# Optimization experiments

Hardware: AMD Instinct MI355X
Metric: run time of the kernel (lower is better)

Reference implementation:

```python
import jax, jax.numpy as jnp
import numpy as np

B, T, E = 2, 2048, 1024
H = 16            # num_heads (global in source repo)
D = E // H        # head_len
LN_EPS = 1e-5


def setup_inputs() -> dict:
    key = jax.random.key(0)
    ks = jax.random.split(key, 12)
    s = lambda fan_in: 1.0 / np.sqrt(fan_in)
    return {
        "x":     jax.random.normal(ks[0], (B, T, E), jnp.float32),
        "ln1_g": jnp.ones((E,), jnp.float32),
        "ln1_b": jnp.zeros((E,), jnp.float32),
        "Wq":    jax.random.normal(ks[1], (E, E), jnp.float32) * s(E),
        "Wk":    jax.random.normal(ks[2], (E, E), jnp.float32) * s(E),
        "Wv":    jax.random.normal(ks[3], (E, E), jnp.float32) * s(E),
        "Wo":    jax.random.normal(ks[4], (E, E), jnp.float32) * s(E),
        "bo":    jnp.zeros((E,), jnp.float32),
        "ln2_g": jnp.ones((E,), jnp.float32),
        "ln2_b": jnp.zeros((E,), jnp.float32),
        "W1":    jax.random.normal(ks[5], (E, 4 * E), jnp.float32) * s(E),
        "b1":    jnp.zeros((4 * E,), jnp.float32),
        "W2":    jax.random.normal(ks[6], (4 * E, E), jnp.float32) * s(4 * E),
        "b2":    jnp.zeros((E,), jnp.float32),
    }


def _layernorm(x, g, b):
    mu = jnp.mean(x, axis=-1, keepdims=True)
    var = jnp.mean(jnp.square(x - mu), axis=-1, keepdims=True)
    return (x - mu) * jax.lax.rsqrt(var + LN_EPS) * g + b


def _attention(x, Wq, Wk, Wv, Wo, bo):
    b, t, e = x.shape
    q = (x @ Wq).reshape(b, t, H, D)
    k = (x @ Wk).reshape(b, t, H, D)
    v = (x @ Wv).reshape(b, t, H, D)
    scores = jnp.einsum("bqhd,bkhd->bhqk", q, k) / np.sqrt(D).astype(np.float32)
    causal = jnp.tril(jnp.ones((t, t), bool))
    scores = jnp.where(causal, scores, -jnp.inf)
    attn = jax.nn.softmax(scores, axis=-1)
    out = jnp.einsum("bhqk,bkhd->bqhd", attn, v).reshape(b, t, e)
    return out @ Wo + bo


def reference(x, ln1_g, ln1_b, Wq, Wk, Wv, Wo, bo, ln2_g, ln2_b, W1, b1, W2, b2):
    # pre-norm attention + residual (dropout=0 / eval mode)
    x = x + _attention(_layernorm(x, ln1_g, ln1_b), Wq, Wk, Wv, Wo, bo)
    # pre-norm MLP + residual
    h = _layernorm(x, ln2_g, ln2_b)
    h = jax.nn.relu(h @ W1 + b1) @ W2 + b2
    return x + h
```

## Files before the change

kernel.cpp:

```cpp
#include <hip/hip_runtime.h>
#include <cmath>
#include <cstdint>
#include <cstddef>

typedef __bf16 bf16_t;
typedef __bf16 bf16x8 __attribute__((ext_vector_type(8)));
typedef float  f32x4  __attribute__((ext_vector_type(4)));

#define B_   2
#define T_   2048
#define E_   1024
#define H_   16
#define D_   64
#define FF_  4096
#define NROW (B_ * T_)
#define QS_  (3 * E_)
#define NTI  (T_ / 64)

__global__ __launch_bounds__(256) void ln_kernel(
    const float* __restrict__ x, const float* __restrict__ g,
    const float* __restrict__ bta, bf16_t* __restrict__ out)
{
    int row = blockIdx.x;
    int tid = threadIdx.x;
    const float4* xr = (const float4*)(x + (size_t)row * E_);
    float4 v = xr[tid];
    float s  = v.x + v.y + v.z + v.w;
    float ss = v.x * v.x + v.y * v.y + v.z * v.z + v.w * v.w;
#pragma unroll
    for (int off = 32; off; off >>= 1) {
        s  += __shfl_xor(s, off);
        ss += __shfl_xor(ss, off);
    }
    __shared__ float red[8];
    int wave = tid >> 6, lane = tid & 63;
    if (lane == 0) { red[wave] = s; red[4 + wave] = ss; }
    __syncthreads();
    s  = red[0] + red[1] + red[2] + red[3];
    ss = red[4] + red[5] + red[6] + red[7];
    float mu   = s * (1.0f / E_);
    float var  = ss * (1.0f / E_) - mu * mu;
    float rstd = rsqrtf(var + 1e-5f);
    float4 gv = ((const float4*)g)[tid];
    float4 bv = ((const float4*)bta)[tid];
    union { bf16_t h[4]; ushort4 u; } pk;
    pk.h[0] = (bf16_t)((v.x - mu) * rstd * gv.x + bv.x);
    pk.h[1] = (bf16_t)((v.y - mu) * rstd * gv.y + bv.y);
    pk.h[2] = (bf16_t)((v.z - mu) * rstd * gv.z + bv.z);
    pk.h[3] = (bf16_t)((v.w - mu) * rstd * gv.w + bv.w);
    ((ushort4*)(out + (size_t)row * E_))[tid] = pk.u;
}

__global__ __launch_bounds__(256) void ln_reduce2(
    const float* __restrict__ p, const float* __restrict__ bias,
    const float* __restrict__ resid, float* __restrict__ x1,
    const float* __restrict__ g, const float* __restrict__ bta,
    bf16_t* __restrict__ out)
{
    int row = blockIdx.x;
    int tid = threadIdx.x;
    size_t off = (size_t)row * E_;
    float4 v0 = ((const float4*)(p + off))[tid];
    float4 v1 = ((const float4*)(p + (size_t)NROW * E_ + off))[tid];
    float4 bb = ((const float4*)bias)[tid];
    float4 rr = ((const float4*)(resid + off))[tid];
    float4 v;
    v.x = v0.x + v1.x + bb.x + rr.x;
    v.y = v0.y + v1.y + bb.y + rr.y;
    v.z = v0.z + v1.z + bb.z + rr.z;
    v.w = v0.w + v1.w + bb.w + rr.w;
    ((float4*)(x1 + off))[tid] = v;
    float s  = v.x + v.y + v.z + v.w;
    float ss = v.x * v.x + v.y * v.y + v.z * v.z + v.w * v.w;
#pragma unroll
    for (int o = 32; o; o >>= 1) {
        s  += __shfl_xor(s, o);
        ss += __shfl_xor(ss, o);
    }
    __shared__ float red[8];
    int wave = tid >> 6, lane = tid & 63;
    if (lane == 0) { red[wave] = s; red[4 + wave] = ss; }
    __syncthreads();
    s  = red[0] + red[1] + red[2] + red[3];
    ss = red[4] + red[5] + red[6] + red[7];
    float mu   = s * (1.0f / E_);
    float var  = ss * (1.0f / E_) - mu * mu;
    float rstd = rsqrtf(var + 1e-5f);
    float4 gv = ((const float4*)g)[tid];
    float4 bv = ((const float4*)bta)[tid];
    union { bf16_t h[4]; ushort4 u; } pk;
    pk.h[0] = (bf16_t)((v.x - mu) * rstd * gv.x + bv.x);
    pk.h[1] = (bf16_t)((v.y - mu) * rstd * gv.y + bv.y);
    pk.h[2] = (bf16_t)((v.z - mu) * rstd * gv.z + bv.z);
    pk.h[3] = (bf16_t)((v.w - mu) * rstd * gv.w + bv.w);
    ((ushort4*)(out + off))[tid] = pk.u;
}

__global__ __launch_bounds__(256) void add_reduce4(
    const float* __restrict__ p, const float* __restrict__ bias,
    const float* __restrict__ resid, float* __restrict__ out)
{
    int row = blockIdx.x;
    int tid = threadIdx.x;
    size_t off = (size_t)row * E_;
    const size_t MN = (size_t)NROW * E_;
    float4 v0 = ((const float4*)(p + off))[tid];
    float4 v1 = ((const float4*)(p + MN + off))[tid];
    float4 v2 = ((const float4*)(p + 2 * MN + off))[tid];
    float4 v3 = ((const float4*)(p + 3 * MN + off))[tid];
    float4 bb = ((const float4*)bias)[tid];
    float4 rr = ((const float4*)(resid + off))[tid];
    float4 v;
    v.x = (v0.x + v1.x) + (v2.x + v3.x) + bb.x + rr.x;
    v.y = (v0.y + v1.y) + (v2.y + v3.y) + bb.y + rr.y;
    v.z = (v0.z + v1.z) + (v2.z + v3.z) + bb.z + rr.z;
    v.w = (v0.w + v1.w) + (v2.w + v3.w) + bb.w + rr.w;
    ((float4*)(out + off))[tid] = v;
}

__global__ __launch_bounds__(256) void transpose_all(
    const float* __restrict__ Wq, const float* __restrict__ Wk,
    const float* __restrict__ Wv, const float* __restrict__ Wo,
    const float* __restrict__ W1, const float* __restrict__ W2,
    bf16_t* __restrict__ wqkv, bf16_t* __restrict__ wot,
    bf16_t* __restrict__ w1t, bf16_t* __restrict__ w2t)
{
    int l = blockIdx.x;
    const float* W; bf16_t* Wt; int K, N, bx, by;
    if (l < 4096) {
        int seg = l >> 10, r = l & 1023;
        K = E_; N = E_; bx = r & 31; by = r >> 5;
        if      (seg == 0) { W = Wq; Wt = wqkv; }
        else if (seg == 1) { W = Wk; Wt = wqkv + (size_t)E_ * E_; }
        else if (seg == 2) { W = Wv; Wt = wqkv + (size_t)2 * E_ * E_; }
        else               { W = Wo; Wt = wot; }
    } else if (l < 8192) {
        int r = l - 4096; K = E_; N = FF_; bx = r & 127; by = r >> 7;
        W = W1; Wt = w1t;
    } else {
        int r = l - 8192; K = FF_; N = E_; bx = r & 31; by = r >> 5;
        W = W2; Wt = w2t;
    }
    __shared__ float t[32][33];
    int n0 = bx * 32, k0 = by * 32;
    int tx = threadIdx.x & 31, ty = threadIdx.x >> 5;
#pragma unroll
    for (int i = 0; i < 4; ++i)
        t[ty + i * 8][tx] = W[(size_t)(k0 + ty + i * 8) * N + n0 + tx];
    __syncthreads();
#pragma unroll
    for (int i = 0; i < 4; ++i)
        Wt[(size_t)(n0 + ty + i * 8) * K + k0 + tx] = (bf16_t)t[tx][ty + i * 8];
}

__device__ __forceinline__ void gload16(const bf16_t* g, bf16_t* l)
{
    __builtin_amdgcn_global_load_lds(
        (const __attribute__((address_space(1))) void*)g,
        (__attribute__((address_space(3))) void*)l, 16, 0, 0);
}

#define BM 128
#define BN 128
#define BK 64

__global__ __launch_bounds__(256) void gemm_bt(
    const bf16_t* __restrict__ A, const bf16_t* __restrict__ Bt,
    const float* __restrict__ bias, const float* __restrict__ resid,
    void* __restrict__ Cout, bf16_t* __restrict__ vt_out,
    int M, int N, int K, int lda, int ldb,
    int has_bias, int do_relu, int has_resid, int out_bf16)
{
    __shared__ __attribute__((aligned(16))) bf16_t As[BM * BK];
    __shared__ __attribute__((aligned(16))) bf16_t Bs[BN * BK];
    int tid  = threadIdx.x;
    int lane = tid & 63, wave = tid >> 6;
    int m0 = blockIdx.x * BM, n0 = blockIdx.y * BN;
    int wm = (wave & 1) * 64, wn = (wave >> 1) * 64;
    int koff = blockIdx.z * K;
    f32x4 acc[4][4];
#pragma unroll
    for (int i = 0; i < 4; ++i)
#pragma unroll
        for (int j = 0; j < 4; ++j) acc[i][j] = (f32x4){0.f, 0.f, 0.f, 0.f};

    const int ml = lane & 15;
    const int g  = lane >> 4;
    const int swl = ml & 7;

    int r8 = lane >> 3;
    int scw = ((lane & 7) ^ r8) * 8;
    const bf16_t* Ag = A  + (size_t)(m0 + wave * 32 + r8) * lda + koff + scw;
    const bf16_t* Bg = Bt + (size_t)(n0 + wave * 32 + r8) * ldb + koff + scw;
    bf16_t* Asw = &As[wave * 32 * BK];
    bf16_t* Bsw = &Bs[wave * 32 * BK];
    int niter = K / BK;

#pragma unroll
    for (int j = 0; j < 4; ++j) {
        gload16(Ag + (size_t)j * 8 * lda, Asw + j * 8 * BK);
        gload16(Bg + (size_t)j * 8 * ldb, Bsw + j * 8 * BK);
    }

    const char* Ac = (const char*)As;
    const char* Bc = (const char*)Bs;
    for (int it = 0; it < niter; ++it) {
        __syncthreads();
#pragma unroll
        for (int ks = 0; ks < 2; ++ks) {
            int swc = (((ks << 2) + g) ^ swl) << 4;
            bf16x8 af[4], bfr[4];
#pragma unroll
            for (int mi = 0; mi < 4; ++mi)
                af[mi] = *(const bf16x8*)(Ac + (wm + mi * 16 + ml) * 128 + swc);
#pragma unroll
            for (int ni = 0; ni < 4; ++ni)
                bfr[ni] = *(const bf16x8*)(Bc + (wn + ni * 16 + ml) * 128 + swc);
#pragma unroll
            for (int mi = 0; mi < 4; ++mi)
#pragma unroll
                for (int ni = 0; ni < 4; ++ni)
                    acc[mi][ni] = __builtin_amdgcn_mfma_f32_16x16x32_bf16(
                        af[mi], bfr[ni], acc[mi][ni], 0, 0, 0);
        }
        if (it + 1 < niter) {
            __syncthreads();
            int k0 = (it + 1) * BK;
#pragma unroll
            for (int j = 0; j < 4; ++j) {
                gload16(Ag + k0 + (size_t)j * 8 * lda, Asw + j * 8 * BK);
                gload16(Bg + k0 + (size_t)j * 8 * ldb, Bsw + j * 8 * BK);
            }
        }
    }

    int r4 = (lane >> 4) * 4;
    if (gridDim.z > 1) {
        float* P = (float*)Cout + (size_t)blockIdx.z * M * N;
#pragma unroll
        for (int mi = 0; mi < 4; ++mi)
#pragma unroll
            for (int ni = 0; ni < 4; ++ni) {
                int col = n0 + wn + ni * 16 + ml;
#pragma unroll
                for (int r = 0; r < 4; ++r) {
                    int row = m0 + wm + mi * 16 + r4 + r;
                    P[(size_t)row * N + col] = acc[mi][ni][r];
                }
            }
        return;
    }
#pragma unroll
    for (int mi = 0; mi < 4; ++mi) {
#pragma unroll
        for (int ni = 0; ni < 4; ++ni) {
            int col = n0 + wn + ni * 16 + ml;
            float bval = has_bias ? bias[col] : 0.0f;
#pragma unroll
            for (int r = 0; r < 4; ++r) {
                int row = m0 + wm + mi * 16 + r4 + r;
                float v = acc[mi][ni][r] + bval;
                if (do_relu)   v = fmaxf(v, 0.0f);
                if (has_resid) v += resid[(size_t)row * N + col];
                if (out_bf16)
                    ((bf16_t*)Cout)[(size_t)row * N + col] = (bf16_t)v;
                else
                    ((float*)Cout)[(size_t)row * N + col] = v;
            }
        }
    }
}

__device__ __forceinline__ void g256_stage_half(
    const bf16_t* gbase, int ldg, bf16_t* lhalf, int wave, int lane)
{
    int r = lane >> 3, c = lane & 7;
    int sc = (c ^ r) * 8;
#pragma unroll
    for (int j = 0; j < 2; ++j) {
        const bf16_t* src = gbase + (size_t)(wave * 8 + j * 64 + r) * ldg + sc;
        bf16_t* dst = lhalf + (wave * 8 + j * 64) * 64;
        __builtin_amdgcn_global_load_lds(
            (const __attribute__((address_space(1))) void*)src,
            (__attribute__((address_space(3))) void*)dst, 16, 0, 0);
    }
}

__device__ __forceinline__ bf16x8 g256_frag(const bf16_t* half, int row, int kb)
{
    return *(const bf16x8*)((const char*)half + row * 128 + (kb ^ ((row & 7) << 4)));
}

template<int FP, bool DO_BFR>
__device__ __forceinline__ void g256_reads(
    const bf16_t* Ahx, const bf16_t* Bhx,
    bf16x8 (&af)[2][2], bf16x8 (&bfr)[4][2],
    int ml, int kq16, int brow0)
{
    if (DO_BFR) {
#pragma unroll
        for (int ni = 0; ni < 4; ++ni) {
            bfr[ni][0] = g256_frag(Bhx, brow0 + ni * 16 + ml, kq16);
            bfr[ni][1] = g256_frag(Bhx, brow0 + ni * 16 + ml, 64 + kq16);
        }
    }
#pragma unroll
    for (int i = 0; i < 2; ++i) {
        af[i][0] = g256_frag(Ahx, (2 * FP + i) * 16 + ml, kq16);
        af[i][1] = g256_frag(Ahx, (2 * FP + i) * 16 + ml, 64 + kq16);
    }
}

template<int FP>
__device__ __forceinline__ void g256_mfma(
    const bf16x8 (&af)[2][2], const bf16x8 (&bfr)[4][2], f32x4 (&acc)[8][4])
{
    __builtin_amdgcn_s_setprio(1);
#pragma unroll
    for (int i = 0; i < 2; ++i)
#pragma unroll
        for (int ni = 0; ni < 4; ++ni)
#pragma unroll
            for (int ks = 0; ks < 2; ++ks)
                acc[2 * FP + i][ni] = __builtin_amdgcn_mfma_f32_16x16x32_bf16(
                    af[i][ks], bfr[ni][ks], acc[2 * FP + i][ni], 0, 0, 0);
    __builtin_amdgcn_s_setprio(0);
}

#define AHALF(t, h) (ldsr + ((((t) & 1) * 4 + (h)) * (128 * 64)))
#define BHALF(t, h) (ldsr + ((((t) & 1) * 4 + 2 + (h)) * (128 * 64)))
#define STG_A(t, h) g256_stage_half(Ab + (size_t)((h) * 128) * lda + (t) * 64, lda, AHALF(t, h), wave, lane)
#define STG_B(t, h) g256_stage_half(Bb + (size_t)((h) * 128) * ldb + (t) * 64, ldb, BHALF(t, h), wave, lane)
#define SBAR() __builtin_amdgcn_s_barrier()

__global__ __launch_bounds__(512, 2) void gemm256(
    const bf16_t* __restrict__ A, const bf16_t* __restrict__ Bt,
    const float* __restrict__ bias,
    void* __restrict__ Cout, bf16_t* __restrict__ vt_out,
    int M, int N, int K, int lda, int ldb,
    int has_bias, int do_relu, int split)
{
    extern __shared__ __attribute__((aligned(16))) bf16_t ldsr[];
    int tid = threadIdx.x, lane = tid & 63, wave = tid >> 6;
    int m0 = blockIdx.x * 256, n0 = blockIdx.y * 256;
    int koff = blockIdx.z * K;
    int ml = lane & 15, kq16 = (lane >> 4) * 16, r4 = (lane >> 4) * 4;
    int wr = (wave >> 2) * 128, wc = (wave & 3) * 64;
    int brow0 = (wave & 1) * 64;

    const bf16_t* Ab = A  + (size_t)m0 * lda + koff;
    const bf16_t* Bb = Bt + (size_t)n0 * ldb + koff;

    const bf16_t* A0 = AHALF(0, wave >> 2);
    const bf16_t* A1 = AHALF(1, wave >> 2);
    const bf16_t* B0 = BHALF(0, (wave & 3) >> 1);
    const bf16_t* B1 = BHALF(1, (wave & 3) >> 1);

    f32x4 acc[8][4];
#pragma unroll
    for (int i = 0; i < 8; ++i)
#pragma unroll
        for (int j = 0; j < 4; ++j) acc[i][j] = (f32x4){0.f, 0.f, 0.f, 0.f};
    bf16x8 bfr[4][2];

    STG_B(0, 0); STG_B(0, 1);
    STG_A(0, 0); STG_A(0, 1);
    STG_B(1, 0); STG_B(1, 1);
    asm volatile("s_waitcnt vmcnt(4)" ::: "memory");
    SBAR();

    int NIT2 = K / 128;
    for (int it = 0; it < NIT2; ++it) {
        bool last = (it == NIT2 - 1);
        int t1 = 2 * it + 1, t2 = 2 * it + 2, t3 = 2 * it + 3;
        bf16x8 af[2][2];

        g256_reads<0, true>(A0, B0, af, bfr, ml, kq16, brow0);
        STG_A(t1, 0);
        SBAR();
        g256_mfma<0>(af, bfr, acc);
        SBAR();

        g256_reads<1, false>(A0, B0, af, bfr, ml, kq16, brow0);
        STG_A(t1, 1);
        SBAR();
        g256_mfma<1>(af, bfr, acc);
        SBAR();

        g256_reads<2, false>(A0, B0, af, bfr, ml, kq16, brow0);
        if (!last) STG_B(t2, 0);
        SBAR();
        g256_mfma<2>(af, bfr, acc);
        SBAR();

        g256_reads<3, false>(A0, B0, af, bfr, ml, kq16, brow0);
        if (!last) STG_B(t2, 1);
        SBAR();
        g256_mfma<3>(af, bfr, acc);
        if (last) asm volatile("s_waitcnt vmcnt(0)" ::: "memory");
        else      asm volatile("s_waitcnt vmcnt(4)" ::: "memory");
        SBAR();

        g256_reads<0, true>(A1, B1, af, bfr, ml, kq16, brow0);
        if (!last) STG_A(t2, 0);
        SBAR();
        g256_mfma<0>(af, bfr, acc);
        SBAR();

        g256_reads<1, false>(A1, B1, af, bfr, ml, kq16, brow0);
        if (!last) STG_A(t2, 1);
        SBAR();
        g256_mfma<1>(af, bfr, acc);
        SBAR();

        g256_reads<2, false>(A1, B1, af, bfr, ml, kq16, brow0);
        if (!last) STG_B(t3, 0);
        SBAR();
        g256_mfma<2>(af, bfr, acc);
        SBAR();

        g256_reads<3, false>(A1, B1, af, bfr, ml, kq16, brow0);
        if (!last) STG_B(t3, 1);
        SBAR();
        g256_mfma<3>(af, bfr, acc);
        if (!last) asm volatile("s_waitcnt vmcnt(4)" ::: "memory");
        SBAR();
    }

    if (split > 1) {
        float* P = (float*)Cout + (size_t)blockIdx.z * M * N;
#pragma unroll
        for (int mi = 0; mi < 8; ++mi)
#pragma unroll
            for (int ni = 0; ni < 4; ++ni) {
                int col = n0 + wc + ni * 16 + ml;
#pragma unroll
                for (int r = 0; r < 4; ++r) {
                    int row = m0 + wr + mi * 16 + r4 + r;
                    P[(size_t)row * N + col] = acc[mi][ni][r];
                }
            }
        return;
    }
    if (vt_out && n0 >= 2 * E_) {
#pragma unroll
        for (int mi = 0; mi < 8; ++mi)
#pragma unroll
            for (int ni = 0; ni < 4; ++ni) {
                int vcol = n0 + wc + ni * 16 + ml - 2 * E_;
                int h = vcol >> 6, d = vcol & 63;
                int row0 = m0 + wr + mi * 16 + r4;
                int b = row0 >> 11, t = row0 & (T_ - 1);
                union { bf16_t h4[4]; uint2 u; } pk;
#pragma unroll
                for (int r = 0; r < 4; ++r) pk.h4[r] = (bf16_t)acc[mi][ni][r];
                *(uint2*)&vt_out[((size_t)(b * H_ + h) * D_ + d) * T_ + t] = pk.u;
            }
        return;
    }
#pragma unroll
    for (int mi = 0; mi < 8; ++mi) {
#pragma unroll
        for (int ni = 0; ni < 4; ++ni) {
            int col = n0 + wc + ni * 16 + ml;
            float bval = has_bias ? bias[col] : 0.0f;
#pragma unroll
            for (int r = 0; r < 4; ++r) {
                int row = m0 + wr + mi * 16 + r4 + r;
                float v = acc[mi][ni][r] + bval;
                if (do_relu) v = fmaxf(v, 0.0f);
                ((bf16_t*)Cout)[(size_t)row * N + col] = (bf16_t)v;
            }
        }
    }
}

#define PSTR 72

struct TileState {
    f32x4 acc[4];
    float m1, l1;
};

__device__ __forceinline__ void attn_stage(
    const bf16_t* kb, const bf16_t* vb,
    bf16_t* ksl, bf16_t* vsl, int wave, int lane)
{
    int r = lane >> 3;
    int sc = ((lane & 7) ^ r) * 8;
#pragma unroll
    for (int j = 0; j < 2; ++j) {
        int rb = wave * 16 + j * 8;
        gload16(kb + (size_t)(rb + r) * QS_ + sc, ksl + rb * 64);
        gload16(vb + (size_t)(rb + r) * T_  + sc, vsl + rb * 64);
    }
}

__device__ __forceinline__ void tile_update(
    const bf16x8 kf[2][4], const bf16x8 vf[2][4], const bf16x8 qf[2],
    TileState& st, bf16_t* PsW, int ml, int r4, int kq8,
    bool diag, int ch, int qrow)
{
    f32x4 s[4];
    __builtin_amdgcn_s_setprio(1);
#pragma unroll
    for (int nt = 0; nt < 4; ++nt) {
        s[nt] = (f32x4){0.f, 0.f, 0.f, 0.f};
#pragma unroll
        for (int ks = 0; ks < 2; ++ks)
            s[nt] = __builtin_amdgcn_mfma_f32_16x16x32_bf16(kf[ks][nt], qf[ks], s[nt], 0, 0, 0);
    }
    __builtin_amdgcn_s_setprio(0);
    if (diag) {
#pragma unroll
        for (int nt = 0; nt < 4; ++nt)
#pragma unroll
            for (int r = 0; r < 4; ++r)
                if (ch * 64 + nt * 16 + r4 + r > qrow) s[nt][r] = -INFINITY;
    }
    float t0 = fmaxf(fmaxf(s[0][0], s[0][1]), s[0][2]);
    float t1 = fmaxf(fmaxf(s[0][3], s[1][0]), s[1][1]);
    float t2 = fmaxf(fmaxf(s[1][2], s[1][3]), s[2][0]);
    float t3 = fmaxf(fmaxf(s[2][1], s[2][2]), s[2][3]);
    float t4 = fmaxf(fmaxf(s[3][0], s[3][1]), s[3][2]);
    float mx = fmaxf(fmaxf(fmaxf(t0, t1), t2),
                     fmaxf(fmaxf(t3, t4), s[3][3]));
    mx = fmaxf(mx, __shfl_xor(mx, 16));
    mx = fmaxf(mx, __shfl_xor(mx, 32));
    if (!__all(mx - st.m1 <= 8.0f)) {
        float mn = fmaxf(st.m1, mx);
        float al = __expf(st.m1 - mn);
        st.m1 = mn;
        st.l1 *= al;
#pragma unroll
        for (int dt = 0; dt < 4; ++dt)
#pragma unroll
            for (int r = 0; r < 4; ++r) st.acc[dt][r] *= al;
    }
    float sum = 0.f;
#pragma unroll
    for (int nt = 0; nt < 4; ++nt)
#pragma unroll
        for (int r = 0; r < 4; ++r) {
            float p = __expf(s[nt][r] - st.m1);
            s[nt][r] = p;
            sum += p;
        }
    sum += __shfl_xor(sum, 16);
    sum += __shfl_xor(sum, 32);
    st.l1 += sum;

#pragma unroll
    for (int nt = 0; nt < 4; ++nt) {
        union { bf16_t h[4]; uint2 u; } pk;
#pragma unroll
        for (int r = 0; r < 4; ++r) pk.h[r] = (bf16_t)s[nt][r];
        *(uint2*)&PsW[ml * PSTR + nt * 16 + r4] = pk.u;
    }
    __builtin_amdgcn_s_setprio(1);
#pragma unroll
    for (int ks = 0; ks < 2; ++ks) {
        bf16x8 pf = *(const bf16x8*)&PsW[ml * PSTR + ks * 32 + kq8];
#pragma unroll
        for (int dt = 0; dt < 4; ++dt)
            st.acc[dt] = __builtin_amdgcn_mfma_f32_16x16x32_bf16(vf[ks][dt], pf, st.acc[dt], 0, 0, 0);
    }
    __builtin_amdgcn_s_setprio(0);
}

__global__ __launch_bounds__(256) void attn_mfma(
    const bf16_t* __restrict__ Qp, const bf16_t* __restrict__ Kp,
    const bf16_t* __restrict__ Vt, bf16_t* __restrict__ O)
{
    __shared__ __attribute__((aligned(16))) bf16_t Ks[2][64 * 64];
    __shared__ __attribute__((aligned(16))) bf16_t Vts[2][64 * 64];
    __shared__ __attribute__((aligned(16))) bf16_t Ps[8][16 * PSTR];

    int tid = threadIdx.x, lane = tid & 63, wave = tid >> 6;
    int ml  = lane & 15;
    int kq8 = (lane >> 4) * 8;
    int g   = lane >> 4;
    int r4  = (lane >> 4) * 4;
    int swl = ml & 7;
    int bh = blockIdx.y, b = bh >> 4, h = bh & 15;
    size_t qk_base = (size_t)b * T_ * QS_ + h * D_;
    size_t vt_base = (size_t)bh * D_ * T_;
    size_t o_base  = (size_t)b * T_ * E_ + h * D_;

    int lo = blockIdx.x, hi = NTI - 1 - blockIdx.x;
    int qlo = lo * 64 + wave * 16;
    int qhi = hi * 64 + wave * 16;

    bf16x8 qfl[2], qfh[2];
#pragma unroll
    for (int ks = 0; ks < 2; ++ks) {
        bf16x8 a = *(const bf16x8*)&Qp[qk_base + (size_t)(qlo + ml) * QS_ + ks * 32 + kq8];
        bf16x8 c = *(const bf16x8*)&Qp[qk_base + (size_t)(qhi + ml) * QS_ + ks * 32 + kq8];
#pragma unroll
        for (int j = 0; j < 8; ++j) {
            a[j] = (bf16_t)((float)a[j] * 0.125f);
            c[j] = (bf16_t)((float)c[j] * 0.125f);
        }
        qfl[ks] = a; qfh[ks] = c;
    }

    TileState stl, sth;
#pragma unroll
    for (int dt = 0; dt < 4; ++dt) {
        stl.acc[dt] = (f32x4){0.f, 0.f, 0.f, 0.f};
        sth.acc[dt] = (f32x4){0.f, 0.f, 0.f, 0.f};
    }
    stl.m1 = -INFINITY; stl.l1 = 0.f;
    sth.m1 = -INFINITY; sth.l1 = 0.f;

    int nch = hi + 1;

    attn_stage(Kp + qk_base, Vt + vt_base, Ks[0], Vts[0], wave, lane);

    for (int ch = 0; ch < nch; ++ch) {
        int cur = ch & 1, nxt = cur ^ 1;
        __syncthreads();

        if (ch + 1 < nch)
            attn_stage(Kp + qk_base + (size_t)((ch + 1) * 64) * QS_,
                       Vt + vt_base + (ch + 1) * 64,
                       Ks[nxt], Vts[nxt], wave, lane);

        bf16x8 kf[2][4], vf[2][4];
        const char* kc = (const char*)Ks[cur];
        const char* vc = (const char*)Vts[cur];
#pragma unroll
        for (int ks = 0; ks < 2; ++ks) {
            int swc = (((ks << 2) + g) ^ swl) << 4;
#pragma unroll
            for (int nt = 0; nt < 4; ++nt) {
                int off = (nt * 16 + ml) * 128 + swc;
                kf[ks][nt] = *(const bf16x8*)(kc + off);
                vf[ks][nt] = *(const bf16x8*)(vc + off);
            }
        }

        tile_update(kf, vf, qfh, sth, Ps[wave], ml, r4, kq8,
                    ch == hi, ch, qhi + ml);
        if (ch <= lo)
            tile_update(kf, vf, qfl, stl, Ps[wave + 4], ml, r4, kq8,
                        ch == lo, ch, qlo + ml);
    }

#pragma unroll
    for (int t = 0; t < 2; ++t) {
        TileState& st = t ? stl : sth;
        int qw = t ? qlo : qhi;
        bf16_t* PsW = Ps[wave + (t ? 4 : 0)];
        float inv = 1.0f / st.l1;
#pragma unroll
        for (int dt = 0; dt < 4; ++dt) {
            union { bf16_t h[4]; uint2 u; } pk;
#pragma unroll
            for (int r = 0; r < 4; ++r) pk.h[r] = (bf16_t)(st.acc[dt][r] * inv);
            *(uint2*)&PsW[ml * PSTR + dt * 16 + r4] = pk.u;
        }
        int row = lane >> 2, seg = (lane & 3) * 16;
        bf16x8 o0 = *(const bf16x8*)&PsW[row * PSTR + seg];
        bf16x8 o1 = *(const bf16x8*)&PsW[row * PSTR + seg + 8];
        size_t gp = o_base + (size_t)(qw + row) * E_ + seg;
        *(bf16x8*)&O[gp]     = o0;
        *(bf16x8*)&O[gp + 8] = o1;
    }
}

extern "C" void kernel_launch(void* const* d_in, const int* in_sizes, int n_in,
                              void* d_out, int out_size, void* d_ws, size_t ws_size,
                              hipStream_t stream)
{
    const float* x    = (const float*)d_in[0];
    const float* ln1g = (const float*)d_in[1];
    const float* ln1b = (const float*)d_in[2];
    const float* Wq   = (const float*)d_in[3];
    const float* Wk   = (const float*)d_in[4];
    const float* Wv   = (const float*)d_in[5];
    const float* Wo   = (const float*)d_in[6];
    const float* bo   = (const float*)d_in[7];
    const float* ln2g = (const float*)d_in[8];
    const float* ln2b = (const float*)d_in[9];
    const float* W1   = (const float*)d_in[10];
    const float* b1   = (const float*)d_in[11];
    const float* W2   = (const float*)d_in[12];
    const float* b2   = (const float*)d_in[13];

    char* ws = (char*)d_ws;
    const size_t MB = 1024ull * 1024ull;
    bf16_t* w2t     = (bf16_t*)(ws + 0 * MB);
    float*  x1      = (float*)(ws + 8 * MB);
    float*  part_wo = (float*)(ws + 24 * MB);
    bf16_t* h1      = (bf16_t*)(ws + 24 * MB);
    bf16_t* w1t     = (bf16_t*)(ws + 56 * MB);
    bf16_t* xn      = (bf16_t*)(ws + 64 * MB);
    bf16_t* hb      = (bf16_t*)(ws + 64 * MB);
    bf16_t* wqkv    = (bf16_t*)(ws + 72 * MB);
    bf16_t* wot     = (bf16_t*)(ws + 78 * MB);
    bf16_t* QKV     = (bf16_t*)(ws + 80 * MB);
    bf16_t* Vtb     = (bf16_t*)(ws + 104 * MB);
    bf16_t* att     = (bf16_t*)(ws + 112 * MB);
    float*  part4   = (float*)(ws + 56 * MB);

    dim3 blk(256), blk5(512);
    const size_t LDS256 = 8 * 128 * 64 * sizeof(bf16_t);

    transpose_all<<<dim3(12288), blk, 0, stream>>>(
        Wq, Wk, Wv, Wo, W1, W2, wqkv, wot, w1t, w2t);

    ln_kernel<<<dim3(NROW), blk, 0, stream>>>(x, ln1g, ln1b, xn);

    gemm256<<<dim3(NROW / 256, QS_ / 256, 1), blk5, LDS256, stream>>>(
        xn, wqkv, nullptr, QKV, Vtb, NROW, QS_, E_, E_, E_, 0, 0, 1);

    attn_mfma<<<dim3(NTI / 2, B_ * H_), blk, 0, stream>>>(
        QKV, QKV + E_, Vtb, att);

    gemm_bt<<<dim3(NROW / BM, E_ / BN, 2), blk, 0, stream>>>(
        att, wot, nullptr, nullptr, part_wo, nullptr, NROW, E_, E_ / 2, E_, E_, 0, 0, 0, 0);
    ln_reduce2<<<dim3(NROW), blk, 0, stream>>>(
        part_wo, bo, x, x1, ln2g, ln2b, hb);

    gemm256<<<dim3(NROW / 256, FF_ / 256, 1), blk5, LDS256, stream>>>(
        hb, w1t, b1, h1, nullptr, NROW, FF_, E_, E_, E_, 1, 1, 1);

    gemm256<<<dim3(NROW / 256, E_ / 256, 4), blk5, LDS256, stream>>>(
        h1, w2t, nullptr, part4, nullptr, NROW, E_, FF_ / 4, FF_, FF_, 0, 0, 4);
    add_reduce4<<<dim3(NROW), blk, 0, stream>>>(
        part4, b2, x1, (float*)d_out);
}
```

Baseline: 329.7 us.

## Split attention q-tile pair across 8 waves and use exp2 softmax

The attention kernel now launches 512 threads per block. Waves 0-3 handle the high q-tile and waves 4-7 handle the low q-tile, instead of each wave processing both tiles serially. Each wave also loads half as many K/V rows per stage. Q is pre-scaled by log2(e)/sqrt(D) so that exp2f can replace __expf. This aims to increase wave-level parallelism and cut per-wave register state, but the low-tile waves sit idle through the barriers on later chunks.

After: 330.4 us. No clear change (+0.2%).

```diff
diff --git a/kernel.cpp b/kernel.cpp
--- a/kernel.cpp
+++ b/kernel.cpp
@@ -476,24 +476,22 @@
 }
 
 #define PSTR 72
+#define QSCL 0.1803368801111204f
 
 struct TileState {
     f32x4 acc[4];
     float m1, l1;
 };
 
-__device__ __forceinline__ void attn_stage(
+__device__ __forceinline__ void attn_stage8(
     const bf16_t* kb, const bf16_t* vb,
     bf16_t* ksl, bf16_t* vsl, int wave, int lane)
 {
     int r = lane >> 3;
     int sc = ((lane & 7) ^ r) * 8;
-#pragma unroll
-    for (int j = 0; j < 2; ++j) {
-        int rb = wave * 16 + j * 8;
-        gload16(kb + (size_t)(rb + r) * QS_ + sc, ksl + rb * 64);
-        gload16(vb + (size_t)(rb + r) * T_  + sc, vsl + rb * 64);
-    }
+    int rb = wave * 8;
+    gload16(kb + (size_t)(rb + r) * QS_ + sc, ksl + rb * 64);
+    gload16(vb + (size_t)(rb + r) * T_  + sc, vsl + rb * 64);
 }
 
 __device__ __forceinline__ void tile_update(
@@ -529,7 +527,7 @@
     mx = fmaxf(mx, __shfl_xor(mx, 32));
     if (!__all(mx - st.m1 <= 8.0f)) {
         float mn = fmaxf(st.m1, mx);
-        float al = __expf(st.m1 - mn);
+        float al = exp2f(st.m1 - mn);
         st.m1 = mn;
         st.l1 *= al;
 #pragma unroll
@@ -542,7 +540,7 @@
     for (int nt = 0; nt < 4; ++nt)
 #pragma unroll
         for (int r = 0; r < 4; ++r) {
-            float p = __expf(s[nt][r] - st.m1);
+            float p = exp2f(s[nt][r] - st.m1);
             s[nt][r] = p;
             sum += p;
         }
@@ -568,7 +566,7 @@
     __builtin_amdgcn_s_setprio(0);
 }
 
-__global__ __launch_bounds__(256) void attn_mfma(
+__global__ __launch_bounds__(512, 4) void attn_mfma(
     const bf16_t* __restrict__ Qp, const bf16_t* __restrict__ Kp,
     const bf16_t* __restrict__ Vt, bf16_t* __restrict__ O)
 {
@@ -588,70 +586,60 @@
     size_t o_base  = (size_t)b * T_ * E_ + h * D_;
 
     int lo = blockIdx.x, hi = NTI - 1 - blockIdx.x;
-    int qlo = lo * 64 + wave * 16;
-    int qhi = hi * 64 + wave * 16;
-
-    bf16x8 qfl[2], qfh[2];
+    int half = wave >> 2, w4 = wave & 3;
+    int qtile = half ? lo : hi;
+    int qw = qtile * 64 + w4 * 16;
+
+    bf16x8 qf[2];
 #pragma unroll
     for (int ks = 0; ks < 2; ++ks) {
-        bf16x8 a = *(const bf16x8*)&Qp[qk_base + (size_t)(qlo + ml) * QS_ + ks * 32 + kq8];
-        bf16x8 c = *(const bf16x8*)&Qp[qk_base + (size_t)(qhi + ml) * QS_ + ks * 32 + kq8];
-#pragma unroll
-        for (int j = 0; j < 8; ++j) {
-            a[j] = (bf16_t)((float)a[j] * 0.125f);
-            c[j] = (bf16_t)((float)c[j] * 0.125f);
-        }
-        qfl[ks] = a; qfh[ks] = c;
-    }
-
-    TileState stl, sth;
-#pragma unroll
-    for (int dt = 0; dt < 4; ++dt) {
-        stl.acc[dt] = (f32x4){0.f, 0.f, 0.f, 0.f};
-        sth.acc[dt] = (f32x4){0.f, 0.f, 0.f, 0.f};
-    }
-    stl.m1 = -INFINITY; stl.l1 = 0.f;
-    sth.m1 = -INFINITY; sth.l1 = 0.f;
+        bf16x8 a = *(const bf16x8*)&Qp[qk_base + (size_t)(qw + ml) * QS_ + ks * 32 + kq8];
+#pragma unroll
+        for (int j = 0; j < 8; ++j)
+            a[j] = (bf16_t)((float)a[j] * QSCL);
+        qf[ks] = a;
+    }
+
+    TileState st;
+#pragma unroll
+    for (int dt = 0; dt < 4; ++dt)
+        st.acc[dt] = (f32x4){0.f, 0.f, 0.f, 0.f};
+    st.m1 = -INFINITY; st.l1 = 0.f;
 
     int nch = hi + 1;
 
-    attn_stage(Kp + qk_base, Vt + vt_base, Ks[0], Vts[0], wave, lane);
+    attn_stage8(Kp + qk_base, Vt + vt_base, Ks[0], Vts[0], wave, lane);
 
     for (int ch = 0; ch < nch; ++ch) {
         int cur = ch & 1, nxt = cur ^ 1;
         __syncthreads();
 
         if (ch + 1 < nch)
-            attn_stage(Kp + qk_base + (size_t)((ch + 1) * 64) * QS_,
-                       Vt + vt_base + (ch + 1) * 64,
-                       Ks[nxt], Vts[nxt], wave, lane);
-
-        bf16x8 kf[2][4], vf[2][4];
-        const char* kc = (const char*)Ks[cur];
-        const char* vc = (const char*)Vts[cur];
-#pragma unroll
-        for (int ks = 0; ks < 2; ++ks) {
-            int swc = (((ks << 2) + g) ^ swl) << 4;
-#pragma unroll
-            for (int nt = 0; nt < 4; ++nt) {
-                int off = (nt * 16 + ml) * 128 + swc;
-                kf[ks][nt] = *(const bf16x8*)(kc + off);
-                vf[ks][nt] = *(const bf16x8*)(vc + off);
+            attn_stage8(Kp + qk_base + (size_t)((ch + 1) * 64) * QS_,
+                        Vt + vt_base + (ch + 1) * 64,
+                        Ks[nxt], Vts[nxt], wave, lane);
+
+        if (ch <= qtile) {
+            bf16x8 kf[2][4], vf[2][4];
+            const char* kc = (const char*)Ks[cur];
+            const char* vc = (const char*)Vts[cur];
+#pragma unroll
+            for (int ks = 0; ks < 2; ++ks) {
+                int swc = (((ks << 2) + g) ^ swl) << 4;
+#pragma unroll
+                for (int nt = 0; nt < 4; ++nt) {
+                    int off = (nt * 16 + ml) * 128 + swc;
+                    kf[ks][nt] = *(const bf16x8*)(kc + off);
+                    vf[ks][nt] = *(const bf16x8*)(vc + off);
+                }
             }
+            tile_update(kf, vf, qf, st, Ps[wave], ml, r4, kq8,
+                        ch == qtile, ch, qw + ml);
         }
-
-        tile_update(kf, vf, qfh, sth, Ps[wave], ml, r4, kq8,
-                    ch == hi, ch, qhi + ml);
-        if (ch <= lo)
-            tile_update(kf, vf, qfl, stl, Ps[wave + 4], ml, r4, kq8,
-                        ch == lo, ch, qlo + ml);
-    }
-
-#pragma unroll
-    for (int t = 0; t < 2; ++t) {
-        TileState& st = t ? stl : sth;
-        int qw = t ? qlo : qhi;
-        bf16_t* PsW = Ps[wave + (t ? 4 : 0)];
+    }
+
+    {
+        bf16_t* PsW = Ps[wave];
         float inv = 1.0f / st.l1;
 #pragma unroll
         for (int dt = 0; dt < 4; ++dt) {
@@ -715,7 +703,7 @@
     gemm256<<<dim3(NROW / 256, QS_ / 256, 1), blk5, LDS256, stream>>>(
         xn, wqkv, nullptr, QKV, Vtb, NROW, QS_, E_, E_, E_, 0, 0, 1);
 
-    attn_mfma<<<dim3(NTI / 2, B_ * H_), blk, 0, stream>>>(
+    attn_mfma<<<dim3(NTI / 2, B_ * H_), dim3(512), 0, stream>>>(
         QKV, QKV + E_, Vtb, att);
 
     gemm_bt<<<dim3(NROW / BM, E_ / BN, 2), blk, 0, stream>>>(
```
